# Optimization experiments

Measured on AMD Instinct MI355X. Metric: run time of the kernel, lower is better.

The kernel has to match this reference:

```python
import jax, jax.numpy as jnp
import numpy as np

N_NODES = 100000
N_EDGES = 1600000
N_GRAPHS = 512
IN_DIM, HID_DIM, OUT_DIM = 128, 256, 128
EPS = 0.0  # PyG GINConv default eps (train_eps=False)


def setup_inputs() -> dict:
    key = jax.random.key(0)
    ks = jax.random.split(key, 9)
    x = jax.random.normal(ks[0], (N_NODES, IN_DIM), dtype=jnp.float32)
    edge_index = jax.random.randint(ks[1], (2, N_EDGES), 0, N_NODES, dtype=jnp.int64)
    batch_ids = jnp.sort(jax.random.randint(ks[2], (N_NODES,), 0, N_GRAPHS, dtype=jnp.int64))
    s1 = 1.0 / np.sqrt(IN_DIM)
    s2 = 1.0 / np.sqrt(HID_DIM)
    W1 = jax.random.normal(ks[3], (IN_DIM, HID_DIM), dtype=jnp.float32) * s1
    b1 = jax.random.normal(ks[4], (HID_DIM,), dtype=jnp.float32) * s1
    W2 = jax.random.normal(ks[5], (HID_DIM, HID_DIM), dtype=jnp.float32) * s2
    b2 = jax.random.normal(ks[6], (HID_DIM,), dtype=jnp.float32) * s2
    Wo = jax.random.normal(ks[7], (HID_DIM, OUT_DIM), dtype=jnp.float32) * s2
    bo = jax.random.normal(ks[8], (OUT_DIM,), dtype=jnp.float32) * s2
    return {"x": x, "edge_index": edge_index, "batch_ids": batch_ids,
            "W1": W1, "b1": b1, "W2": W2, "b2": b2, "Wo": Wo, "bo": bo}


def reference(x, edge_index, batch_ids, W1, b1, W2, b2, Wo, bo):
    src, dst = edge_index[0], edge_index[1]
    # GIN aggregation: sum of neighbor features scattered to destination nodes
    agg = jax.ops.segment_sum(x[src], dst, num_segments=N_NODES)  # [N, in]
    h = (1.0 + EPS) * x + agg
    # GIN MLP: Linear -> ReLU -> Linear -> ReLU
    h = jax.nn.relu(h @ W1 + b1)
    h = jax.nn.relu(h @ W2 + b2)
    out = h @ Wo + bo  # output_layer
    # global_add_pool over graphs
    pooled = jax.ops.segment_sum(out, batch_ids, num_segments=N_GRAPHS)  # [G, out]
    return pooled
```

## Files before the change

### kernel.cpp

```cpp
#include <hip/hip_runtime.h>

#define N_NODES  100000
#define M_PAD    100096
#define N_EDGES  1600000
#define N_GRAPHS 512
#define IN_DIM   128
#define HID_DIM  256
#define OUT_DIM  128

#define NB       782
#define BCAP     3072
#define CHUNK    2048
#define BKB      ((N_EDGES + CHUNK - 1) / CHUNK)

typedef __bf16 bf16x8 __attribute__((ext_vector_type(8)));
typedef __bf16 bf16x4 __attribute__((ext_vector_type(4)));
typedef __bf16 bf16x2 __attribute__((ext_vector_type(2)));
typedef float  f32x4  __attribute__((ext_vector_type(4)));

#define WP_L2_BASE 32768
#define WP_L3_BASE 98304
#define WP_TOTAL   131072

#define R_X    (N_NODES * IN_DIM / 4)
#define R_APAD ((M_PAD - N_NODES) * IN_DIM / 4)
#define R_WP   WP_TOTAL
#define R_OUT  (N_GRAPHS * OUT_DIM / 4)
#define R_TOTAL (R_X + R_APAD + R_WP + R_OUT)
#define NI     ((R_TOTAL + 255) / 256)
#define GRID_IB (BKB + NI)

__global__ __launch_bounds__(256) void init_bucket_kernel(const float* __restrict__ x,
                                                          const float* __restrict__ W1,
                                                          const float* __restrict__ W2,
                                                          const float* __restrict__ Wo,
                                                          const int* __restrict__ ei,
                                                          __bf16* __restrict__ xb,
                                                          __bf16* __restrict__ Apad,
                                                          __bf16* __restrict__ Wp,
                                                          float* __restrict__ outbuf,
                                                          int* __restrict__ gcursor,
                                                          unsigned* __restrict__ pairBuf) {
    __shared__ int lcnt[NB];
    __shared__ int lbase[NB];
    const int tid = threadIdx.x;

    if (blockIdx.x < BKB) {
        const int e0 = blockIdx.x * CHUNK;

        for (int b = tid; b < NB; b += 256) lcnt[b] = 0;
        __syncthreads();

        for (int i = tid; i < CHUNK; i += 256) {
            int e = e0 + i;
            if (e < N_EDGES) atomicAdd(&lcnt[ei[N_EDGES + e] >> 7], 1);
        }
        __syncthreads();

        for (int b = tid; b < NB; b += 256) {
            int c = lcnt[b];
            lbase[b] = c ? atomicAdd(&gcursor[b], c) : 0;
            lcnt[b] = 0;
        }
        __syncthreads();

        for (int i = tid; i < CHUNK; i += 256) {
            int e = e0 + i;
            if (e < N_EDGES) {
                int s = ei[e];
                int d = ei[N_EDGES + e];
                int b = d >> 7;
                int pos = lbase[b] + atomicAdd(&lcnt[b], 1);
                if (pos < BCAP)
                    pairBuf[(size_t)b * BCAP + pos] = (unsigned)s | ((unsigned)(d & 127) << 17);
            }
        }
        return;
    }

    long long i = (long long)(blockIdx.x - BKB) * blockDim.x + tid;
    if (i < R_X) {
        float4 v = ((const float4*)x)[i];
        bf16x4 h;
        h.x = (__bf16)v.x; h.y = (__bf16)v.y; h.z = (__bf16)v.z; h.w = (__bf16)v.w;
        ((bf16x4*)xb)[i] = h;
        return;
    }
    i -= R_X;
    if (i < R_APAD) {
        bf16x4 z; z.x = (__bf16)0.f; z.y = (__bf16)0.f; z.z = (__bf16)0.f; z.w = (__bf16)0.f;
        ((bf16x4*)Apad)[i] = z;
        return;
    }
    i -= R_APAD;
    if (i < R_WP) {
        int idx = (int)i;
        const float* src;
        int K, Nn, base;
        if (idx < WP_L2_BASE)      { src = W1; K = 128; Nn = 256; base = 0; }
        else if (idx < WP_L3_BASE) { src = W2; K = 256; Nn = 256; base = WP_L2_BASE; }
        else                       { src = Wo; K = 256; Nn = 128; base = WP_L3_BASE; }
        int r0 = idx - base;
        int slabElems = 32 * K;
        int j = r0 / slabElems;
        int r = r0 % slabElems;
        int KS = K / 32;
        int p = r >> 9;
        int lane = (r >> 3) & 63;
        int e = r & 7;
        int s = p % KS, t = p / KS;
        int quad = lane >> 4, l16 = lane & 15;
        int n = j * 32 + t * 16 + l16;
        int k = s * 32 + quad * 8 + e;
        Wp[idx] = (__bf16)src[(size_t)k * Nn + n];
        return;
    }
    i -= R_WP;
    if (i < R_OUT) {
        ((float4*)outbuf)[i] = make_float4(0.f, 0.f, 0.f, 0.f);
        return;
    }
}

#define AGG_THREADS 512

__global__ __launch_bounds__(AGG_THREADS) void aggB_kernel(const unsigned* __restrict__ pairBuf,
                                                           const int* __restrict__ gcursor,
                                                           const __bf16* __restrict__ xb,
                                                           __bf16* __restrict__ A) {
    __shared__ int lcnt[128];
    __shared__ int loffs[128];
    __shared__ int lcur[128];
    __shared__ int offx[128];
    __shared__ unsigned sorted[BCAP];

    const int b = blockIdx.x;
    const int tid = threadIdx.x;
    const int node0 = b << 7;
    const int cnt = min(gcursor[b], BCAP);
    const unsigned* pb = pairBuf + (size_t)b * BCAP;

    if (tid < 128) { lcnt[tid] = 0; lcur[tid] = 0; }
    __syncthreads();

    for (int i = tid; i < cnt; i += AGG_THREADS)
        atomicAdd(&lcnt[pb[i] >> 17], 1);
    __syncthreads();

    if (tid < 128) loffs[tid] = lcnt[tid];
    __syncthreads();
    for (int st = 1; st < 128; st <<= 1) {
        int add = (tid < 128 && tid >= st) ? loffs[tid - st] : 0;
        __syncthreads();
        if (tid < 128) loffs[tid] += add;
        __syncthreads();
    }
    if (tid < 128) offx[tid] = loffs[tid] - lcnt[tid];
    __syncthreads();

    for (int i = tid; i < cnt; i += AGG_THREADS) {
        unsigned u = pb[i];
        int dl = u >> 17;
        int slot = atomicAdd(&lcur[dl], 1);
        sorted[offx[dl] + slot] = u & 0x1FFFF;
    }
    __syncthreads();

    const int wid = tid >> 6;
    const int lane = tid & 63;
    const int c0 = lane * 2;

    #pragma unroll 1
    for (int n = wid; n < 128; n += (AGG_THREADS / 64)) {
        int v = node0 + n;
        if (v >= N_NODES) break;
        int off = offx[n];
        int len = lcnt[n];
        bf16x2 self = *(const bf16x2*)(xb + (size_t)v * IN_DIM + c0);
        float ax = (float)self.x, ay = (float)self.y;

        int addr = off + lane;
        if (addr >= cnt) addr = (cnt > 0) ? cnt - 1 : 0;
        int myidx = (int)sorted[addr];

        int lim = len < 64 ? len : 64;
        int j = 0;
        for (; j + 8 <= lim; j += 8) {
            int s0 = __shfl(myidx, j + 0, 64);
            int s1 = __shfl(myidx, j + 1, 64);
            int s2 = __shfl(myidx, j + 2, 64);
            int s3 = __shfl(myidx, j + 3, 64);
            int s4 = __shfl(myidx, j + 4, 64);
            int s5 = __shfl(myidx, j + 5, 64);
            int s6 = __shfl(myidx, j + 6, 64);
            int s7 = __shfl(myidx, j + 7, 64);
            bf16x2 v0 = *(const bf16x2*)(xb + (size_t)s0 * IN_DIM + c0);
            bf16x2 v1 = *(const bf16x2*)(xb + (size_t)s1 * IN_DIM + c0);
            bf16x2 v2 = *(const bf16x2*)(xb + (size_t)s2 * IN_DIM + c0);
            bf16x2 v3 = *(const bf16x2*)(xb + (size_t)s3 * IN_DIM + c0);
            bf16x2 v4 = *(const bf16x2*)(xb + (size_t)s4 * IN_DIM + c0);
            bf16x2 v5 = *(const bf16x2*)(xb + (size_t)s5 * IN_DIM + c0);
            bf16x2 v6 = *(const bf16x2*)(xb + (size_t)s6 * IN_DIM + c0);
            bf16x2 v7 = *(const bf16x2*)(xb + (size_t)s7 * IN_DIM + c0);
            ax += (float)v0.x + (float)v1.x + (float)v2.x + (float)v3.x
                + (float)v4.x + (float)v5.x + (float)v6.x + (float)v7.x;
            ay += (float)v0.y + (float)v1.y + (float)v2.y + (float)v3.y
                + (float)v4.y + (float)v5.y + (float)v6.y + (float)v7.y;
        }
        for (; j < lim; ++j) {
            int s = __shfl(myidx, j, 64);
            bf16x2 vv = *(const bf16x2*)(xb + (size_t)s * IN_DIM + c0);
            ax += (float)vv.x;
            ay += (float)vv.y;
        }
        for (; j < len; ++j) {
            int s = (int)sorted[off + j];
            bf16x2 vv = *(const bf16x2*)(xb + (size_t)s * IN_DIM + c0);
            ax += (float)vv.x;
            ay += (float)vv.y;
        }
        bf16x2 h;
        h.x = (__bf16)ax;
        h.y = (__bf16)ay;
        *(bf16x2*)(A + (size_t)v * IN_DIM + c0) = h;
    }
}

__device__ __forceinline__ void load_group_p(const __bf16* __restrict__ p, int lane,
                                             bf16x8* __restrict__ dst) {
    #pragma unroll
    for (int e = 0; e < 8; ++e)
        dst[e] = *(const bf16x8*)(p + (e * 64 + lane) * 8);
}

__device__ __forceinline__ void store_H(__bf16* __restrict__ H, int j, int quad, int l16,
                                        const f32x4 (&acc)[2][2], float bt0, float bt1) {
    const int c7 = l16 & 7;
    const int ch = l16 >> 3;
    #pragma unroll
    for (int i = 0; i < 2; ++i)
        #pragma unroll
        for (int t = 0; t < 2; ++t) {
            const float bb = t ? bt1 : bt0;
            #pragma unroll
            for (int rr = 0; rr < 4; ++rr) {
                int row = i * 16 + quad * 4 + rr;
                int cidx = (j * 4 + t * 2 + ch + row) & 31;
                float v = fmaxf(acc[i][t][rr] + bb, 0.f);
                H[row * 256 + cidx * 8 + c7] = (__bf16)v;
            }
        }
}

__global__ __launch_bounds__(64) void mlp_fused(const __bf16* __restrict__ A,
                                                const __bf16* __restrict__ Wp,
                                                const float* __restrict__ b1,
                                                const float* __restrict__ b2,
                                                const float* __restrict__ bo,
                                                float* __restrict__ out,
                                                const int* __restrict__ batch) {
    __shared__ __bf16 H[32 * 256];

    const int lane = threadIdx.x;
    const int quad = lane >> 4, l16 = lane & 15;
    const size_t mblk = (size_t)blockIdx.x * 32;
    const int r0g = (int)mblk;
    int gfirst = (r0g < N_NODES) ? batch[r0g] : -2;
    int glast  = (r0g + 31 < N_NODES) ? batch[r0g + 31] : -1;

    bf16x8 a[2][8];
    bf16x8 buf0[8];
    bf16x8 buf1[8];

    const __bf16* wp = Wp;
    load_group_p(wp, lane, buf0);

    #pragma unroll
    for (int i = 0; i < 2; ++i)
        #pragma unroll
        for (int s = 0; s < 4; ++s)
            a[i][s] = *(const bf16x8*)(A + (mblk + i * 16 + l16) * IN_DIM + s * 32 + quad * 8);

    #pragma unroll 1
    for (int j = 0; j < 8; j += 2) {
        {
            load_group_p(wp + 4096, lane, buf1);
            float bt0 = b1[j * 32 + l16];
            float bt1 = b1[j * 32 + 16 + l16];
            f32x4 acc[2][2] = {};
            #pragma unroll
            for (int p = 0; p < 8; ++p) {
                const int t = p >> 2, s = p & 3;
                acc[0][t] = __builtin_amdgcn_mfma_f32_16x16x32_bf16(a[0][s], buf0[p], acc[0][t], 0, 0, 0);
                acc[1][t] = __builtin_amdgcn_mfma_f32_16x16x32_bf16(a[1][s], buf0[p], acc[1][t], 0, 0, 0);
            }
            store_H(H, j, quad, l16, acc, bt0, bt1);
        }
        {
            load_group_p(wp + 8192, lane, buf0);
            float bt0 = b1[(j + 1) * 32 + l16];
            float bt1 = b1[(j + 1) * 32 + 16 + l16];
            f32x4 acc[2][2] = {};
            #pragma unroll
            for (int p = 0; p < 8; ++p) {
                const int t = p >> 2, s = p & 3;
                acc[0][t] = __builtin_amdgcn_mfma_f32_16x16x32_bf16(a[0][s], buf1[p], acc[0][t], 0, 0, 0);
                acc[1][t] = __builtin_amdgcn_mfma_f32_16x16x32_bf16(a[1][s], buf1[p], acc[1][t], 0, 0, 0);
            }
            store_H(H, j + 1, quad, l16, acc, bt0, bt1);
        }
        wp += 8192;
    }
    __syncthreads();

    #pragma unroll
    for (int i = 0; i < 2; ++i)
        #pragma unroll
        for (int s = 0; s < 8; ++s) {
            int row = i * 16 + l16;
            a[i][s] = *(const bf16x8*)(H + row * 256 + (((s * 4 + quad) + row) & 31) * 8);
        }
    __syncthreads();

    #pragma unroll 1
    for (int j = 0; j < 8; ++j) {
        load_group_p(wp + 4096, lane, buf1);
        float bt0 = b2[j * 32 + l16];
        float bt1 = b2[j * 32 + 16 + l16];
        f32x4 acc[2][2] = {};
        #pragma unroll
        for (int p = 0; p < 8; ++p) {
            acc[0][0] = __builtin_amdgcn_mfma_f32_16x16x32_bf16(a[0][p], buf0[p], acc[0][0], 0, 0, 0);
            acc[1][0] = __builtin_amdgcn_mfma_f32_16x16x32_bf16(a[1][p], buf0[p], acc[1][0], 0, 0, 0);
        }
        load_group_p(wp + 8192, lane, buf0);
        #pragma unroll
        for (int p = 0; p < 8; ++p) {
            acc[0][1] = __builtin_amdgcn_mfma_f32_16x16x32_bf16(a[0][p], buf1[p], acc[0][1], 0, 0, 0);
            acc[1][1] = __builtin_amdgcn_mfma_f32_16x16x32_bf16(a[1][p], buf1[p], acc[1][1], 0, 0, 0);
        }
        store_H(H, j, quad, l16, acc, bt0, bt1);
        wp += 8192;
    }
    __syncthreads();

    #pragma unroll
    for (int i = 0; i < 2; ++i)
        #pragma unroll
        for (int s = 0; s < 8; ++s) {
            int row = i * 16 + l16;
            a[i][s] = *(const bf16x8*)(H + row * 256 + (((s * 4 + quad) + row) & 31) * 8);
        }

    #pragma unroll 1
    for (int j = 0; j < 4; ++j) {
        load_group_p(wp + 4096, lane, buf1);
        float bt0 = bo[j * 32 + l16];
        float bt1 = bo[j * 32 + 16 + l16];
        f32x4 acc[2][2] = {};
        #pragma unroll
        for (int p = 0; p < 8; ++p) {
            acc[0][0] = __builtin_amdgcn_mfma_f32_16x16x32_bf16(a[0][p], buf0[p], acc[0][0], 0, 0, 0);
            acc[1][0] = __builtin_amdgcn_mfma_f32_16x16x32_bf16(a[1][p], buf0[p], acc[1][0], 0, 0, 0);
        }
        load_group_p(wp + 8192, lane, buf0);
        #pragma unroll
        for (int p = 0; p < 8; ++p) {
            acc[0][1] = __builtin_amdgcn_mfma_f32_16x16x32_bf16(a[0][p], buf1[p], acc[0][1], 0, 0, 0);
            acc[1][1] = __builtin_amdgcn_mfma_f32_16x16x32_bf16(a[1][p], buf1[p], acc[1][1], 0, 0, 0);
        }

        if (gfirst == glast) {
            #pragma unroll
            for (int t = 0; t < 2; ++t) {
                float sum = 0.f;
                #pragma unroll
                for (int i = 0; i < 2; ++i)
                    #pragma unroll
                    for (int rr = 0; rr < 4; ++rr) sum += acc[i][t][rr];
                sum += __shfl_xor(sum, 16, 64);
                sum += __shfl_xor(sum, 32, 64);
                if (quad == 0) {
                    int c = j * 32 + t * 16 + l16;
                    float bb = t ? bt1 : bt0;
                    atomicAdd(out + (size_t)gfirst * OUT_DIM + c, sum + 32.f * bb);
                }
            }
        } else {
            #pragma unroll
            for (int i = 0; i < 2; ++i)
                #pragma unroll
                for (int rr = 0; rr < 4; ++rr) {
                    int m = r0g + i * 16 + quad * 4 + rr;
                    if (m < N_NODES) {
                        int g = batch[m];
                        #pragma unroll
                        for (int t = 0; t < 2; ++t) {
                            int c = j * 32 + t * 16 + l16;
                            float bb = t ? bt1 : bt0;
                            atomicAdd(out + (size_t)g * OUT_DIM + c, acc[i][t][rr] + bb);
                        }
                    }
                }
        }
        wp += 8192;
    }
}

extern "C" void kernel_launch(void* const* d_in, const int* in_sizes, int n_in,
                              void* d_out, int out_size, void* d_ws, size_t ws_size,
                              hipStream_t stream) {
    const float* x  = (const float*)d_in[0];
    const int*   ei = (const int*)d_in[1];
    const int*   bi = (const int*)d_in[2];
    const float* W1 = (const float*)d_in[3];
    const float* b1 = (const float*)d_in[4];
    const float* W2 = (const float*)d_in[5];
    const float* b2 = (const float*)d_in[6];
    const float* Wo = (const float*)d_in[7];
    const float* bo = (const float*)d_in[8];
    float* out = (float*)d_out;

    __bf16* A  = (__bf16*)d_ws;
    __bf16* xb = A + (size_t)M_PAD * IN_DIM;
    __bf16* Wp = xb + (size_t)N_NODES * IN_DIM;
    unsigned* pairBuf = (unsigned*)(Wp + WP_TOTAL);
    int* gcursor  = (int*)(pairBuf + (size_t)NB * BCAP);

    hipMemsetAsync(gcursor, 0, NB * sizeof(int), stream);

    init_bucket_kernel<<<GRID_IB, 256, 0, stream>>>(
        x, W1, W2, Wo, ei, xb, A + (size_t)N_NODES * IN_DIM, Wp, out, gcursor, pairBuf);

    aggB_kernel<<<NB, AGG_THREADS, 0, stream>>>(pairBuf, gcursor, xb, A);

    mlp_fused<<<M_PAD / 32, 64, 0, stream>>>(A, Wp, b1, b2, bo, out, bi);
}
```

Before: 278.2 us.

## Fuse bucketed aggregation and MLP into one kernel via shared-memory tile

Merges the aggregation kernel and the fused MLP kernel so each 128-node bucket block aggregates neighbour features into a swizzled shared-memory tile. Four waves then run the three-layer MLP on 32-row slices of that tile, and the intermediate A matrix in global memory and its zero padding go away. The intent is to save the global write and read of A and one kernel launch. In exchange the block uses 64KB of shared memory and drops from 512 to 256 threads, which lowers occupancy and may serialise the gather and MFMA phases within a block.

After: 373.4 us. 1.34x slower.

```diff
diff --git a/kernel.cpp b/kernel.cpp
--- a/kernel.cpp
+++ b/kernel.cpp
@@ -23,10 +23,9 @@
 #define WP_TOTAL   131072
 
 #define R_X    (N_NODES * IN_DIM / 4)
-#define R_APAD ((M_PAD - N_NODES) * IN_DIM / 4)
 #define R_WP   WP_TOTAL
 #define R_OUT  (N_GRAPHS * OUT_DIM / 4)
-#define R_TOTAL (R_X + R_APAD + R_WP + R_OUT)
+#define R_TOTAL (R_X + R_WP + R_OUT)
 #define NI     ((R_TOTAL + 255) / 256)
 #define GRID_IB (BKB + NI)
 
@@ -36,7 +35,6 @@
                                                           const float* __restrict__ Wo,
                                                           const int* __restrict__ ei,
                                                           __bf16* __restrict__ xb,
-                                                          __bf16* __restrict__ Apad,
                                                           __bf16* __restrict__ Wp,
                                                           float* __restrict__ outbuf,
                                                           int* __restrict__ gcursor,
@@ -87,12 +85,6 @@
         return;
     }
     i -= R_X;
-    if (i < R_APAD) {
-        bf16x4 z; z.x = (__bf16)0.f; z.y = (__bf16)0.f; z.z = (__bf16)0.f; z.w = (__bf16)0.f;
-        ((bf16x4*)Apad)[i] = z;
-        return;
-    }
-    i -= R_APAD;
     if (i < R_WP) {
         int idx = (int)i;
         const float* src;
@@ -122,17 +114,49 @@
     }
 }
 
-#define AGG_THREADS 512
-
-__global__ __launch_bounds__(AGG_THREADS) void aggB_kernel(const unsigned* __restrict__ pairBuf,
+__device__ __forceinline__ void load_group_p(const __bf16* __restrict__ p, int lane,
+                                             bf16x8* __restrict__ dst) {
+    #pragma unroll
+    for (int e = 0; e < 8; ++e)
+        dst[e] = *(const bf16x8*)(p + (e * 64 + lane) * 8);
+}
+
+__device__ __forceinline__ void store_H(__bf16* __restrict__ H, int j, int quad, int l16,
+                                        const f32x4 (&acc)[2][2], float bt0, float bt1) {
+    const int c7 = l16 & 7;
+    const int ch = l16 >> 3;
+    #pragma unroll
+    for (int i = 0; i < 2; ++i)
+        #pragma unroll
+        for (int t = 0; t < 2; ++t) {
+            const float bb = t ? bt1 : bt0;
+            #pragma unroll
+            for (int rr = 0; rr < 4; ++rr) {
+                int row = i * 16 + quad * 4 + rr;
+                int cidx = (j * 4 + t * 2 + ch + row) & 31;
+                float v = fmaxf(acc[i][t][rr] + bb, 0.f);
+                H[row * 256 + cidx * 8 + c7] = (__bf16)v;
+            }
+        }
+}
+
+#define BF_THREADS 256
+
+__global__ __launch_bounds__(BF_THREADS) void bucket_fused(const unsigned* __restrict__ pairBuf,
                                                            const int* __restrict__ gcursor,
                                                            const __bf16* __restrict__ xb,
-                                                           __bf16* __restrict__ A) {
-    __shared__ int lcnt[128];
-    __shared__ int loffs[128];
-    __shared__ int lcur[128];
-    __shared__ int offx[128];
-    __shared__ unsigned sorted[BCAP];
+                                                           const __bf16* __restrict__ Wp,
+                                                           const float* __restrict__ b1,
+                                                           const float* __restrict__ b2,
+                                                           const float* __restrict__ bo,
+                                                           float* __restrict__ out,
+                                                           const int* __restrict__ batch) {
+    __shared__ __align__(16) char smem[65536];
+    unsigned* sorted = (unsigned*)(smem + 32768);
+    int* lcnt  = (int*)(smem + 45056);
+    int* loffs = lcnt + 128;
+    int* lcur  = loffs + 128;
+    int* offx  = lcur + 128;
 
     const int b = blockIdx.x;
     const int tid = threadIdx.x;
@@ -143,7 +167,7 @@
     if (tid < 128) { lcnt[tid] = 0; lcur[tid] = 0; }
     __syncthreads();
 
-    for (int i = tid; i < cnt; i += AGG_THREADS)
+    for (int i = tid; i < cnt; i += BF_THREADS)
         atomicAdd(&lcnt[pb[i] >> 17], 1);
     __syncthreads();
 
@@ -158,7 +182,7 @@
     if (tid < 128) offx[tid] = loffs[tid] - lcnt[tid];
     __syncthreads();
 
-    for (int i = tid; i < cnt; i += AGG_THREADS) {
+    for (int i = tid; i < cnt; i += BF_THREADS) {
         unsigned u = pb[i];
         int dl = u >> 17;
         int slot = atomicAdd(&lcur[dl], 1);
@@ -169,11 +193,17 @@
     const int wid = tid >> 6;
     const int lane = tid & 63;
     const int c0 = lane * 2;
+    const int c0b = lane * 4;
 
     #pragma unroll 1
-    for (int n = wid; n < 128; n += (AGG_THREADS / 64)) {
+    for (int n = wid; n < 128; n += 4) {
         int v = node0 + n;
-        if (v >= N_NODES) break;
+        char* dstp = smem + n * 256 + (c0b ^ ((n & 7) << 4));
+        if (v >= N_NODES) {
+            bf16x2 z; z.x = (__bf16)0.f; z.y = (__bf16)0.f;
+            *(bf16x2*)dstp = z;
+            continue;
+        }
         int off = offx[n];
         int len = lcnt[n];
         bf16x2 self = *(const bf16x2*)(xb + (size_t)v * IN_DIM + c0);
@@ -222,64 +252,31 @@
         bf16x2 h;
         h.x = (__bf16)ax;
         h.y = (__bf16)ay;
-        *(bf16x2*)(A + (size_t)v * IN_DIM + c0) = h;
-    }
-}
-
-__device__ __forceinline__ void load_group_p(const __bf16* __restrict__ p, int lane,
-                                             bf16x8* __restrict__ dst) {
-    #pragma unroll
-    for (int e = 0; e < 8; ++e)
-        dst[e] = *(const bf16x8*)(p + (e * 64 + lane) * 8);
-}
-
-__device__ __forceinline__ void store_H(__bf16* __restrict__ H, int j, int quad, int l16,
-                                        const f32x4 (&acc)[2][2], float bt0, float bt1) {
-    const int c7 = l16 & 7;
-    const int ch = l16 >> 3;
+        *(bf16x2*)dstp = h;
+    }
+    __syncthreads();
+
+    const int quad = lane >> 4, l16 = lane & 15;
+    __bf16* Hw = (__bf16*)(smem + wid * 16384);
+    const int r0g = node0 + wid * 32;
+    int gfirst = (r0g < N_NODES) ? batch[r0g] : -2;
+    int glast  = (r0g + 31 < N_NODES) ? batch[r0g + 31] : -1;
+
+    bf16x8 a[2][8];
     #pragma unroll
     for (int i = 0; i < 2; ++i)
         #pragma unroll
-        for (int t = 0; t < 2; ++t) {
-            const float bb = t ? bt1 : bt0;
-            #pragma unroll
-            for (int rr = 0; rr < 4; ++rr) {
-                int row = i * 16 + quad * 4 + rr;
-                int cidx = (j * 4 + t * 2 + ch + row) & 31;
-                float v = fmaxf(acc[i][t][rr] + bb, 0.f);
-                H[row * 256 + cidx * 8 + c7] = (__bf16)v;
-            }
-        }
-}
-
-__global__ __launch_bounds__(64) void mlp_fused(const __bf16* __restrict__ A,
-                                                const __bf16* __restrict__ Wp,
-                                                const float* __restrict__ b1,
-                                                const float* __restrict__ b2,
-                                                const float* __restrict__ bo,
-                                                float* __restrict__ out,
-                                                const int* __restrict__ batch) {
-    __shared__ __bf16 H[32 * 256];
-
-    const int lane = threadIdx.x;
-    const int quad = lane >> 4, l16 = lane & 15;
-    const size_t mblk = (size_t)blockIdx.x * 32;
-    const int r0g = (int)mblk;
-    int gfirst = (r0g < N_NODES) ? batch[r0g] : -2;
-    int glast  = (r0g + 31 < N_NODES) ? batch[r0g + 31] : -1;
-
-    bf16x8 a[2][8];
+        for (int s = 0; s < 4; ++s) {
+            int lrow = wid * 32 + i * 16 + l16;
+            a[i][s] = *(const bf16x8*)(smem + lrow * 256 +
+                                       ((s * 64 + quad * 16) ^ ((lrow & 7) << 4)));
+        }
+    __syncthreads();
+
     bf16x8 buf0[8];
     bf16x8 buf1[8];
-
     const __bf16* wp = Wp;
     load_group_p(wp, lane, buf0);
-
-    #pragma unroll
-    for (int i = 0; i < 2; ++i)
-        #pragma unroll
-        for (int s = 0; s < 4; ++s)
-            a[i][s] = *(const bf16x8*)(A + (mblk + i * 16 + l16) * IN_DIM + s * 32 + quad * 8);
 
     #pragma unroll 1
     for (int j = 0; j < 8; j += 2) {
@@ -294,7 +291,7 @@
                 acc[0][t] = __builtin_amdgcn_mfma_f32_16x16x32_bf16(a[0][s], buf0[p], acc[0][t], 0, 0, 0);
                 acc[1][t] = __builtin_amdgcn_mfma_f32_16x16x32_bf16(a[1][s], buf0[p], acc[1][t], 0, 0, 0);
             }
-            store_H(H, j, quad, l16, acc, bt0, bt1);
+            store_H(Hw, j, quad, l16, acc, bt0, bt1);
         }
         {
             load_group_p(wp + 8192, lane, buf0);
@@ -307,7 +304,7 @@
                 acc[0][t] = __builtin_amdgcn_mfma_f32_16x16x32_bf16(a[0][s], buf1[p], acc[0][t], 0, 0, 0);
                 acc[1][t] = __builtin_amdgcn_mfma_f32_16x16x32_bf16(a[1][s], buf1[p], acc[1][t], 0, 0, 0);
             }
-            store_H(H, j + 1, quad, l16, acc, bt0, bt1);
+            store_H(Hw, j + 1, quad, l16, acc, bt0, bt1);
         }
         wp += 8192;
     }
@@ -318,7 +315,7 @@
         #pragma unroll
         for (int s = 0; s < 8; ++s) {
             int row = i * 16 + l16;
-            a[i][s] = *(const bf16x8*)(H + row * 256 + (((s * 4 + quad) + row) & 31) * 8);
+            a[i][s] = *(const bf16x8*)(Hw + row * 256 + (((s * 4 + quad) + row) & 31) * 8);
         }
     __syncthreads();
 
@@ -339,7 +336,7 @@
             acc[0][1] = __builtin_amdgcn_mfma_f32_16x16x32_bf16(a[0][p], buf1[p], acc[0][1], 0, 0, 0);
             acc[1][1] = __builtin_amdgcn_mfma_f32_16x16x32_bf16(a[1][p], buf1[p], acc[1][1], 0, 0, 0);
         }
-        store_H(H, j, quad, l16, acc, bt0, bt1);
+        store_H(Hw, j, quad, l16, acc, bt0, bt1);
         wp += 8192;
     }
     __syncthreads();
@@ -349,7 +346,7 @@
         #pragma unroll
         for (int s = 0; s < 8; ++s) {
             int row = i * 16 + l16;
-            a[i][s] = *(const bf16x8*)(H + row * 256 + (((s * 4 + quad) + row) & 31) * 8);
+            a[i][s] = *(const bf16x8*)(Hw + row * 256 + (((s * 4 + quad) + row) & 31) * 8);
         }
 
     #pragma unroll 1
@@ -421,8 +418,7 @@
     const float* bo = (const float*)d_in[8];
     float* out = (float*)d_out;
 
-    __bf16* A  = (__bf16*)d_ws;
-    __bf16* xb = A + (size_t)M_PAD * IN_DIM;
+    __bf16* xb = (__bf16*)d_ws;
     __bf16* Wp = xb + (size_t)N_NODES * IN_DIM;
     unsigned* pairBuf = (unsigned*)(Wp + WP_TOTAL);
     int* gcursor  = (int*)(pairBuf + (size_t)NB * BCAP);
@@ -430,9 +426,8 @@
     hipMemsetAsync(gcursor, 0, NB * sizeof(int), stream);
 
     init_bucket_kernel<<<GRID_IB, 256, 0, stream>>>(
-        x, W1, W2, Wo, ei, xb, A + (size_t)N_NODES * IN_DIM, Wp, out, gcursor, pairBuf);
-
-    aggB_kernel<<<NB, AGG_THREADS, 0, stream>>>(pairBuf, gcursor, xb, A);
-
-    mlp_fused<<<M_PAD / 32, 64, 0, stream>>>(A, Wp, b1, b2, bo, out, bi);
+        x, W1, W2, Wo, ei, xb, Wp, out, gcursor, pairBuf);
+
+    bucket_fused<<<NB, BF_THREADS, 0, stream>>>(
+        pairBuf, gcursor, xb, Wp, b1, b2, bo, out, bi);
 }
```
